# Kernel tuning notes

Hardware: AMD Instinct MI355X
Metric: run time of the kernel (lower is better)

Reference implementation:

```python
import jax, jax.numpy as jnp
import numpy as np

BN_EPS = 1e-5
STRIDE = 12          # ACCENT_DOWNSAMPLE_STRIDE
NQ = 8               # ACCENT_VQ_QUANTIZERS
K = 256              # ACCENT_VQ_CODEBOOK_SIZE
VQ_D = 16            # ACCENT_VQ_DIM
EMB = 128            # ACCENT_EMBEDDING_DIM


def conv1d(x, w, b, stride=1, padding=0):
    # x: (B, Cin, T), w: (Cout, Cin, Kw)
    y = jax.lax.conv_general_dilated(
        x, w, window_strides=(stride,), padding=[(padding, padding)],
        dimension_numbers=("NCW", "OIW", "NCW"))
    return y + b[None, :, None]


def batchnorm(x, gamma, beta, mean, var):
    # eval-mode BatchNorm1d over channel dim
    inv = jax.lax.rsqrt(var + BN_EPS)
    return (x - mean[None, :, None]) * (inv * gamma)[None, :, None] + beta[None, :, None]


def setup_inputs() -> dict:
    key = jax.random.key(0)
    ks = jax.random.split(key, 12)
    C = 256
    d = {
        "mel_spectrogram": jax.random.normal(ks[0], (16, 80, 4096), jnp.float32),
        "w1": jax.random.normal(ks[1], (C, 80, 5), jnp.float32) * 0.05,
        "b1": jnp.zeros((C,), jnp.float32),
        "g1": jnp.ones((C,), jnp.float32),
        "be1": jnp.zeros((C,), jnp.float32),
        "m1": jax.random.normal(ks[2], (C,), jnp.float32) * 0.1,
        "v1": jax.random.uniform(ks[3], (C,), jnp.float32, 0.5, 1.5),
        "w2": jax.random.normal(ks[4], (C, C, 5), jnp.float32) * 0.03,
        "b2": jnp.zeros((C,), jnp.float32),
        "g2": jnp.ones((C,), jnp.float32),
        "be2": jnp.zeros((C,), jnp.float32),
        "m2": jax.random.normal(ks[5], (C,), jnp.float32) * 0.1,
        "v2": jax.random.uniform(ks[6], (C,), jnp.float32, 0.5, 1.5),
        "wd": jax.random.normal(ks[7], (EMB, C, 2 * STRIDE), jnp.float32) * 0.02,
        "bd": jnp.zeros((EMB,), jnp.float32),
        "wp": jax.random.normal(ks[8], (VQ_D, EMB, 1), jnp.float32) * 0.1,
        "bp": jnp.zeros((VQ_D,), jnp.float32),
        "codebooks": jax.random.normal(ks[9], (NQ, K, VQ_D), jnp.float32) * 0.3,
    }
    return d


def reference(mel_spectrogram, w1, b1, g1, be1, m1, v1,
              w2, b2, g2, be2, m2, v2, wd, bd, wp, bp, codebooks):
    # CNN stack
    x = jax.nn.relu(batchnorm(conv1d(mel_spectrogram, w1, b1, 1, 2), g1, be1, m1, v1))
    x = jax.nn.relu(batchnorm(conv1d(x, w2, b2, 1, 2), g2, be2, m2, v2))
    # Downsample conv: kernel=24, stride=12, pad=6
    e_a_unq = conv1d(x, wd, bd, STRIDE, STRIDE // 2)          # (B, 128, T')
    z = conv1d(e_a_unq, wp, bp, 1, 0)                          # (B, 16, T')
    # RVQ: 8 sequential cdist-argmin-subtract steps
    r = jnp.transpose(z, (0, 2, 1))                            # (B, T', 16)
    idx_list = []
    for q in range(NQ):
        cb = codebooks[q]                                      # (K, 16)
        # squared euclidean distances (B, T', K)
        d = (jnp.sum(r * r, -1, keepdims=True)
             - 2.0 * jnp.einsum("btd,kd->btk", r, cb)
             + jnp.sum(cb * cb, -1))
        idx = jnp.argmin(d, axis=-1)                           # (B, T')
        idx_list.append(idx)
        r = r - cb[idx]                                        # residual update
    indices = jnp.stack(idx_list, axis=0)                      # (NQ, B, T')
    return e_a_unq, indices
```

## Files before the change

kernel.cpp:

```cpp
#include <hip/hip_runtime.h>
#include <math.h>

#define B_    16
#define T_    4096
#define C_    256
#define CIN1  80
#define EMB   128
#define TP    341
#define NPOS  (B_*TP)
#define NQ_   8
#define KCB   256
#define BN_EPS 1e-5

__global__ __launch_bounds__(256) void prep_v7(
    const float* __restrict__ w2, const float* __restrict__ wd,
    const float* __restrict__ b1, const float* __restrict__ g1,
    const float* __restrict__ be1, const float* __restrict__ m1,
    const float* __restrict__ v1,
    const float* __restrict__ b2, const float* __restrict__ g2,
    const float* __restrict__ be2, const float* __restrict__ m2,
    const float* __restrict__ v2,
    float* __restrict__ w2t, float* __restrict__ wdt,
    double* __restrict__ a1, double* __restrict__ bt1,
    double* __restrict__ a2, double* __restrict__ bt2)
{
    int j = blockIdx.x * 256 + threadIdx.x;
    if (j < 256*24*128) wdt[j] = wd[(size_t)(j & 127) * 6144 + (j >> 7)];
    if (j < 256*5*256)  w2t[j] = w2[(size_t)(j & 255) * 1280 + (j >> 8)];
    if (j < 256) {
        double inv1 = 1.0 / sqrt((double)v1[j] + BN_EPS);
        double s1 = (double)g1[j] * inv1;
        a1[j]  = s1;
        bt1[j] = ((double)b1[j] - (double)m1[j]) * s1 + (double)be1[j];
        double inv2 = 1.0 / sqrt((double)v2[j] + BN_EPS);
        double s2 = (double)g2[j] * inv2;
        a2[j]  = s2;
        bt2[j] = ((double)b2[j] - (double)m2[j]) * s2 + (double)be2[j];
    }
}

__device__ __forceinline__ int swz_pair(int col) {
    int bw = col >> 1;
    return ((bw ^ ((bw >> 3) & 7)) << 1);
}
__device__ __forceinline__ int swz_scalar(int col) {
    int bw = col >> 1;
    return (((bw ^ ((bw >> 3) & 7)) << 1) | (col & 1));
}

template<int CIN, typename Tin, bool TR>
__global__ __launch_bounds__(256, 2) void conv5_v8(
    const Tin* __restrict__ in,
    const float* __restrict__ wt,
    const double* __restrict__ alpha, const double* __restrict__ beta,
    double* __restrict__ out)
{
    const int b   = blockIdx.z;
    const int co0 = blockIdx.y * 64;
    const int t0  = blockIdx.x * 256;
    const int tid = threadIdx.x;
    const int tcol = tid & 15;
    const int trow = tid >> 4;

    __shared__ __align__(16) double xs[8][264];
    __shared__ __align__(16) double wsh[40][64];

    double acc[4][16];
    #pragma unroll
    for (int i = 0; i < 4; ++i)
        #pragma unroll
        for (int j = 0; j < 16; ++j) acc[i][j] = 0.0;

    for (int c0 = 0; c0 < CIN; c0 += 8) {
        for (int i = tid; i < 8 * 260; i += 256) {
            int ci = i / 260, col = i - ci * 260;
            int t = t0 - 2 + col;
            double v = 0.0;
            if (t >= 0 && t < T_) v = (double)in[((size_t)(b * CIN + c0 + ci)) * T_ + t];
            xs[ci][swz_scalar(col)] = v;
        }
        for (int i = tid; i < 40 * 64; i += 256) {
            int r = i >> 6, co = i & 63;
            float wv;
            if (TR) wv = wt[(size_t)(c0 * 5 + r) * 256 + co0 + co];
            else    wv = wt[(size_t)(co0 + co) * (CIN * 5) + c0 * 5 + r];
            wsh[r][co] = (double)wv;
        }
        __syncthreads();

        #pragma unroll 2
        for (int ci = 0; ci < 8; ++ci) {
            double wv[20];
            #pragma unroll
            for (int k = 0; k < 5; ++k) {
                double2 wa = *(const double2*)&wsh[ci * 5 + k][trow * 4];
                double2 wb = *(const double2*)&wsh[ci * 5 + k][trow * 4 + 2];
                wv[k * 4 + 0] = wa.x; wv[k * 4 + 1] = wa.y;
                wv[k * 4 + 2] = wb.x; wv[k * 4 + 3] = wb.y;
            }
            #pragma unroll
            for (int h = 0; h < 2; ++h) {
                double xv[12];
                #pragma unroll
                for (int m = 0; m < 6; ++m) {
                    double2 v2 = *(const double2*)&xs[ci][swz_pair(tcol * 16 + h * 8 + 2 * m)];
                    xv[2 * m] = v2.x; xv[2 * m + 1] = v2.y;
                }
                #pragma unroll
                for (int k = 0; k < 5; ++k)
                    #pragma unroll
                    for (int i4 = 0; i4 < 4; ++i4) {
                        double w = wv[k * 4 + i4];
                        #pragma unroll
                        for (int j = 0; j < 8; ++j)
                            acc[i4][h * 8 + j] = fma(w, xv[j + k], acc[i4][h * 8 + j]);
                    }
            }
        }
        __syncthreads();
    }

    const int cobase = co0 + trow * 4;
    const int tg = t0 + tcol * 16;
    #pragma unroll
    for (int i4 = 0; i4 < 4; ++i4) {
        double a = alpha[cobase + i4], bt = beta[cobase + i4];
        size_t base = ((size_t)(b * C_ + cobase + i4)) * T_ + tg;
        #pragma unroll
        for (int m = 0; m < 8; ++m) {
            double2 o;
            double y0 = fma(acc[i4][2 * m], a, bt);
            double y1 = fma(acc[i4][2 * m + 1], a, bt);
            o.x = y0 > 0.0 ? y0 : 0.0;
            o.y = y1 > 0.0 ? y1 : 0.0;
            *(double2*)&out[base + 2 * m] = o;
        }
    }
}

__global__ __launch_bounds__(256, 2) void convd_f64_v7(
    const double* __restrict__ x2,
    const float* __restrict__ wdt,
    double* __restrict__ parts,
    int nb, int nsplit, int cis)
{
    const int bz  = blockIdx.z;
    const int s   = bz % nsplit;
    const int b   = bz / nsplit;
    const int tp0 = blockIdx.x * 128;
    const int tid = threadIdx.x;
    const int tcol = tid & 15;
    const int crow = tid >> 4;

    __shared__ __align__(16) double xs2[24][132];
    __shared__ __align__(16) double wsh[24][128];

    double acc[8][8];
    #pragma unroll
    for (int i = 0; i < 8; ++i)
        #pragma unroll
        for (int j = 0; j < 8; ++j) acc[i][j] = 0.0;

    const int tbase = tp0 * 12 - 6;
    const int ci_begin = s * cis;

    for (int c = ci_begin; c < ci_begin + cis; ++c) {
        for (int i = tid; i < 1548; i += 256) {
            int t = tbase + i;
            double v = (t >= 0 && t < T_)
                ? x2[((size_t)(b * 256 + c)) * T_ + t] : 0.0;
            int tp = (i * 43691) >> 19;
            int kp = i - tp * 12;
            xs2[kp][swz_scalar(tp)] = v;
            if (tp >= 1) xs2[kp + 12][swz_scalar(tp - 1)] = v;
        }
        for (int i = tid; i < 24 * 128; i += 256) {
            int r = i >> 7, cc = i & 127;
            wsh[r][cc] = (double)wdt[((size_t)c * 24 + r) * 128 + cc];
        }
        __syncthreads();

        #pragma unroll 4
        for (int k = 0; k < 24; ++k) {
            double wv[8];
            #pragma unroll
            for (int m = 0; m < 4; ++m) {
                double2 w2v = *(const double2*)&wsh[k][crow * 8 + 2 * m];
                wv[2 * m] = w2v.x; wv[2 * m + 1] = w2v.y;
            }
            #pragma unroll
            for (int jp = 0; jp < 4; ++jp) {
                double2 xp = *(const double2*)&xs2[k][swz_pair(tcol * 2 + 32 * jp)];
                #pragma unroll
                for (int i = 0; i < 8; ++i) {
                    acc[i][jp * 2]     = fma(wv[i], xp.x, acc[i][jp * 2]);
                    acc[i][jp * 2 + 1] = fma(wv[i], xp.y, acc[i][jp * 2 + 1]);
                }
            }
        }
        __syncthreads();
    }

    #pragma unroll
    for (int i = 0; i < 8; ++i) {
        int co = crow * 8 + i;
        #pragma unroll
        for (int jp = 0; jp < 4; ++jp) {
            #pragma unroll
            for (int e = 0; e < 2; ++e) {
                int tp = tp0 + tcol * 2 + 32 * jp + e;
                if (tp < TP)
                    parts[(((size_t)s * nb + b) * EMB + co) * TP + tp] = acc[i][jp * 2 + e];
            }
        }
    }
}

__global__ __launch_bounds__(256) void convd_combine(
    double* __restrict__ parts,
    const float* __restrict__ bd,
    float* __restrict__ e_out,
    int nb, int b_off, int nsplit)
{
    int idx = blockIdx.x * 256 + threadIdx.x;
    int total = nb * EMB * TP;
    if (idx >= total) return;
    int rem = idx % (EMB * TP);
    int co = rem / TP;
    size_t stride = (size_t)nb * EMB * TP;
    double y = 0.0;
    for (int s = 0; s < nsplit; ++s)
        y += parts[(size_t)s * stride + idx];
    y += (double)bd[co];
    parts[idx] = y;
    e_out[(size_t)b_off * EMB * TP + idx] = (float)y;
}

__global__ __launch_bounds__(128) void zproj_f64(
    const double* __restrict__ ed,
    const float* __restrict__ wp,
    const float* __restrict__ bp,
    double* __restrict__ z)
{
    const int b = blockIdx.y;
    const int t = blockIdx.x * 128 + threadIdx.x;
    __shared__ double wps[16][128];
    for (int i = threadIdx.x; i < 16 * 128; i += 128)
        wps[i >> 7][i & 127] = (double)wp[i];
    __syncthreads();
    if (t >= TP) return;
    double acc[16];
    #pragma unroll
    for (int v = 0; v < 16; ++v) acc[v] = (double)bp[v];
    for (int co = 0; co < 128; ++co) {
        double x = ed[((size_t)(b * EMB + co)) * TP + t];
        #pragma unroll
        for (int v = 0; v < 16; ++v) acc[v] = fma(x, wps[v][co], acc[v]);
    }
    #pragma unroll
    for (int v = 0; v < 16; ++v)
        z[((size_t)(b * TP + t)) * 16 + v] = acc[v];
}

__global__ __launch_bounds__(256) void rvq_f64_v2(
    const double* __restrict__ z,
    const float* __restrict__ cb,
    float* __restrict__ out_idx)
{
    const int pos = blockIdx.x;
    const int tid = threadIdx.x;
    const int lane = tid & 63;
    const int wv = tid >> 6;

    __shared__ double r[16];
    __shared__ double wd_s[4];
    __shared__ int wi_s[4];
    __shared__ int best_s;

    if (tid < 16) r[tid] = z[(size_t)pos * 16 + tid];
    __syncthreads();

    for (int q = 0; q < NQ_; ++q) {
        const float* c = cb + ((size_t)(q * KCB) + tid) * 16;
        double d = 0.0;
        #pragma unroll
        for (int i = 0; i < 16; ++i) {
            double diff = r[i] - (double)c[i];
            d = fma(diff, diff, d);
        }
        int idx = tid;
        #pragma unroll
        for (int sft = 32; sft > 0; sft >>= 1) {
            double d2 = __shfl_down(d, sft, 64);
            int i2 = __shfl_down(idx, sft, 64);
            if (d2 < d || (d2 == d && i2 < idx)) { d = d2; idx = i2; }
        }
        if (lane == 0) { wd_s[wv] = d; wi_s[wv] = idx; }
        __syncthreads();
        if (tid == 0) {
            double bd_ = wd_s[0]; int bi = wi_s[0];
            #pragma unroll
            for (int w = 1; w < 4; ++w) {
                if (wd_s[w] < bd_ || (wd_s[w] == bd_ && wi_s[w] < bi)) {
                    bd_ = wd_s[w]; bi = wi_s[w];
                }
            }
            best_s = bi;
            out_idx[(size_t)q * NPOS + pos] = (float)bi;
        }
        __syncthreads();
        int best = best_s;
        if (tid < 16)
            r[tid] = r[tid] - (double)cb[((size_t)(q * KCB) + best) * 16 + tid];
        __syncthreads();
    }
}

extern "C" void kernel_launch(void* const* d_in, const int* in_sizes, int n_in,
                              void* d_out, int out_size, void* d_ws, size_t ws_size,
                              hipStream_t stream) {
    const float* mel = (const float*)d_in[0];
    const float* w1  = (const float*)d_in[1];
    const float* b1  = (const float*)d_in[2];
    const float* g1  = (const float*)d_in[3];
    const float* be1 = (const float*)d_in[4];
    const float* m1  = (const float*)d_in[5];
    const float* v1  = (const float*)d_in[6];
    const float* w2  = (const float*)d_in[7];
    const float* b2  = (const float*)d_in[8];
    const float* g2  = (const float*)d_in[9];
    const float* be2 = (const float*)d_in[10];
    const float* m2  = (const float*)d_in[11];
    const float* v2  = (const float*)d_in[12];
    const float* wd  = (const float*)d_in[13];
    const float* bd  = (const float*)d_in[14];
    const float* wp  = (const float*)d_in[15];
    const float* bp  = (const float*)d_in[16];
    const float* cb  = (const float*)d_in[17];

    const int nb = 8;
    const int ngrp = B_ / nb;
    const int nsplit = 16;
    const int cis = 256 / nsplit;

    auto al = [](size_t x) { return (x + 255) & ~(size_t)255; };
    const size_t x1_big   = (size_t)nb * C_ * T_ * 8;
    const size_t x1_small = (size_t)4  * C_ * T_ * 8;
    const size_t parts_b  = (size_t)nsplit * nb * EMB * TP * 8;
    const size_t x2_bytes = (size_t)nb * C_ * T_ * 8;
    const size_t tail = al((size_t)256*5*256*4)
                      + al((size_t)256*24*128*4)
                      + 4 * al(2048)
                      + al((size_t)B_ * TP * 16 * 8);
    const size_t need_big = al(x1_big) + al(x2_bytes) + tail;

    const bool big = (ws_size >= need_big);
    const int cc = big ? 8 : 4;
    const size_t shared_bytes = big ? x1_big
                                    : (x1_small > parts_b ? x1_small : parts_b);

    char* ws = (char*)d_ws;
    size_t off = 0;
    auto alloc = [&](size_t bytes) -> char* {
        char* p = ws + off;
        off = (off + bytes + 255) & ~(size_t)255;
        return p;
    };
    char* shared = alloc(shared_bytes);
    double* x1d  = (double*)shared;
    double* parts= (double*)shared;
    double* x2d  = (double*)alloc(x2_bytes);
    float*  w2t  = (float*)alloc((size_t)256*5*256*4);
    float*  wdt  = (float*)alloc((size_t)256*24*128*4);
    double* a1d  = (double*)alloc(2048);
    double* bt1d = (double*)alloc(2048);
    double* a2d  = (double*)alloc(2048);
    double* bt2d = (double*)alloc(2048);
    double* zd   = (double*)alloc((size_t)B_ * TP * 16 * 8);

    float* e_out   = (float*)d_out;
    float* idx_out = (float*)d_out + (size_t)B_ * EMB * TP;

    prep_v7<<<3072, 256, 0, stream>>>(w2, wd, b1, g1, be1, m1, v1,
                                      b2, g2, be2, m2, v2,
                                      w2t, wdt, a1d, bt1d, a2d, bt2d);

    const int comb_blocks = (nb * EMB * TP + 255) / 256;
    for (int g = 0; g < ngrp; ++g) {
        for (int ch = 0; ch < nb / cc; ++ch) {
            int b_abs = g * nb + ch * cc;
            conv5_v8<CIN1, float, false>
                <<<dim3(16, 4, cc), 256, 0, stream>>>(
                mel + (size_t)b_abs * CIN1 * T_, w1, a1d, bt1d,
                x1d + (big ? (size_t)ch * cc * C_ * T_ : 0));
            conv5_v8<C_, double, true>
                <<<dim3(16, 4, cc), 256, 0, stream>>>(
                x1d + (big ? (size_t)ch * cc * C_ * T_ : 0), w2t, a2d, bt2d,
                x2d + (size_t)ch * cc * C_ * T_);
        }
        convd_f64_v7<<<dim3(3, 1, nb * nsplit), 256, 0, stream>>>(
            x2d, wdt, parts, nb, nsplit, cis);
        convd_combine<<<comb_blocks, 256, 0, stream>>>(
            parts, bd, e_out, nb, g * nb, nsplit);
        zproj_f64<<<dim3(3, nb), 128, 0, stream>>>(
            parts, wp, bp, zd + (size_t)g * nb * TP * 16);
    }
    rvq_f64_v2<<<NPOS, 256, 0, stream>>>(zd, cb, idx_out);
}
```

Before: 1.781 ms.

## Rewrite conv5 as register-tiled direct-from-global kernel with wave-uniform weights

Replaces the LDS-tiled fp64 conv5 kernel with one that keeps no shared memory. Each wave handles 16 output channels and each lane two time steps, reading inputs straight from global memory. Weights are loaded as wave-uniform (scalar) values from a pre-transposed, optionally fp64-converted copy, so the inner loop avoids per-iteration conversion. The change also raises occupancy to 4 blocks per CU, drops the batch chunking so each conv covers all 8 batches in one launch, and adds a tier that stores weights as double when workspace allows. The cost is less data reuse per thread and heavier reliance on cache for the overlapping input reads.

```diff
diff --git a/kernel.cpp b/kernel.cpp
--- a/kernel.cpp
+++ b/kernel.cpp
@@ -12,21 +12,20 @@
 #define KCB   256
 #define BN_EPS 1e-5
 
-__global__ __launch_bounds__(256) void prep_v7(
-    const float* __restrict__ w2, const float* __restrict__ wd,
+__global__ __launch_bounds__(256) void prep_common(
+    const float* __restrict__ wd,
     const float* __restrict__ b1, const float* __restrict__ g1,
     const float* __restrict__ be1, const float* __restrict__ m1,
     const float* __restrict__ v1,
     const float* __restrict__ b2, const float* __restrict__ g2,
     const float* __restrict__ be2, const float* __restrict__ m2,
     const float* __restrict__ v2,
-    float* __restrict__ w2t, float* __restrict__ wdt,
+    float* __restrict__ wdt,
     double* __restrict__ a1, double* __restrict__ bt1,
     double* __restrict__ a2, double* __restrict__ bt2)
 {
     int j = blockIdx.x * 256 + threadIdx.x;
     if (j < 256*24*128) wdt[j] = wd[(size_t)(j & 127) * 6144 + (j >> 7)];
-    if (j < 256*5*256)  w2t[j] = w2[(size_t)(j & 255) * 1280 + (j >> 8)];
     if (j < 256) {
         double inv1 = 1.0 / sqrt((double)v1[j] + BN_EPS);
         double s1 = (double)g1[j] * inv1;
@@ -39,6 +38,23 @@
     }
 }
 
+__global__ __launch_bounds__(256) void prep_wf64(
+    const float* __restrict__ w1, const float* __restrict__ w2,
+    double* __restrict__ w1td, double* __restrict__ w2td)
+{
+    int j = blockIdx.x * 256 + threadIdx.x;
+    if (j < 256*5*256) w2td[j] = (double)w2[(size_t)(j & 255) * 1280 + (j >> 8)];
+    if (j < 80*5*256)  w1td[j] = (double)w1[(size_t)(j & 255) * 400 + (j >> 8)];
+}
+__global__ __launch_bounds__(256) void prep_wf32(
+    const float* __restrict__ w1, const float* __restrict__ w2,
+    float* __restrict__ w1tf, float* __restrict__ w2tf)
+{
+    int j = blockIdx.x * 256 + threadIdx.x;
+    if (j < 256*5*256) w2tf[j] = w2[(size_t)(j & 255) * 1280 + (j >> 8)];
+    if (j < 80*5*256)  w1tf[j] = w1[(size_t)(j & 255) * 400 + (j >> 8)];
+}
+
 __device__ __forceinline__ int swz_pair(int col) {
     int bw = col >> 1;
     return ((bw ^ ((bw >> 3) & 7)) << 1);
@@ -48,93 +64,62 @@
     return (((bw ^ ((bw >> 3) & 7)) << 1) | (col & 1));
 }
 
-template<int CIN, typename Tin, bool TR>
-__global__ __launch_bounds__(256, 2) void conv5_v8(
+template<int CIN, typename Tin, typename WT>
+__global__ __launch_bounds__(256, 4) void conv5_v10(
     const Tin* __restrict__ in,
-    const float* __restrict__ wt,
+    const WT* __restrict__ wt,
     const double* __restrict__ alpha, const double* __restrict__ beta,
     double* __restrict__ out)
 {
-    const int b   = blockIdx.z;
-    const int co0 = blockIdx.y * 64;
-    const int t0  = blockIdx.x * 256;
-    const int tid = threadIdx.x;
-    const int tcol = tid & 15;
-    const int trow = tid >> 4;
-
-    __shared__ __align__(16) double xs[8][264];
-    __shared__ __align__(16) double wsh[40][64];
-
-    double acc[4][16];
-    #pragma unroll
-    for (int i = 0; i < 4; ++i)
-        #pragma unroll
-        for (int j = 0; j < 16; ++j) acc[i][j] = 0.0;
-
-    for (int c0 = 0; c0 < CIN; c0 += 8) {
-        for (int i = tid; i < 8 * 260; i += 256) {
-            int ci = i / 260, col = i - ci * 260;
-            int t = t0 - 2 + col;
-            double v = 0.0;
-            if (t >= 0 && t < T_) v = (double)in[((size_t)(b * CIN + c0 + ci)) * T_ + t];
-            xs[ci][swz_scalar(col)] = v;
-        }
-        for (int i = tid; i < 40 * 64; i += 256) {
-            int r = i >> 6, co = i & 63;
-            float wv;
-            if (TR) wv = wt[(size_t)(c0 * 5 + r) * 256 + co0 + co];
-            else    wv = wt[(size_t)(co0 + co) * (CIN * 5) + c0 * 5 + r];
-            wsh[r][co] = (double)wv;
-        }
-        __syncthreads();
-
-        #pragma unroll 2
-        for (int ci = 0; ci < 8; ++ci) {
-            double wv[20];
-            #pragma unroll
-            for (int k = 0; k < 5; ++k) {
-                double2 wa = *(const double2*)&wsh[ci * 5 + k][trow * 4];
-                double2 wb = *(const double2*)&wsh[ci * 5 + k][trow * 4 + 2];
-                wv[k * 4 + 0] = wa.x; wv[k * 4 + 1] = wa.y;
-                wv[k * 4 + 2] = wb.x; wv[k * 4 + 3] = wb.y;
-            }
-            #pragma unroll
-            for (int h = 0; h < 2; ++h) {
-                double xv[12];
-                #pragma unroll
-                for (int m = 0; m < 6; ++m) {
-                    double2 v2 = *(const double2*)&xs[ci][swz_pair(tcol * 16 + h * 8 + 2 * m)];
-                    xv[2 * m] = v2.x; xv[2 * m + 1] = v2.y;
-                }
-                #pragma unroll
-                for (int k = 0; k < 5; ++k)
-                    #pragma unroll
-                    for (int i4 = 0; i4 < 4; ++i4) {
-                        double w = wv[k * 4 + i4];
-                        #pragma unroll
-                        for (int j = 0; j < 8; ++j)
-                            acc[i4][h * 8 + j] = fma(w, xv[j + k], acc[i4][h * 8 + j]);
-                    }
-            }
-        }
-        __syncthreads();
-    }
-
-    const int cobase = co0 + trow * 4;
-    const int tg = t0 + tcol * 16;
-    #pragma unroll
-    for (int i4 = 0; i4 < 4; ++i4) {
-        double a = alpha[cobase + i4], bt = beta[cobase + i4];
-        size_t base = ((size_t)(b * C_ + cobase + i4)) * T_ + tg;
-        #pragma unroll
-        for (int m = 0; m < 8; ++m) {
-            double2 o;
-            double y0 = fma(acc[i4][2 * m], a, bt);
-            double y1 = fma(acc[i4][2 * m + 1], a, bt);
-            o.x = y0 > 0.0 ? y0 : 0.0;
-            o.y = y1 > 0.0 ? y1 : 0.0;
-            *(double2*)&out[base + 2 * m] = o;
-        }
+    const int b  = blockIdx.z;
+    const int t0 = blockIdx.y * 128;
+    const int wv = __builtin_amdgcn_readfirstlane((int)(threadIdx.x >> 6));
+    const int lane = threadIdx.x & 63;
+    const int co0 = blockIdx.x * 64 + wv * 16;
+    const int t = t0 + lane * 2;
+
+    double acc[16][2];
+    #pragma unroll
+    for (int c = 0; c < 16; ++c) { acc[c][0] = 0.0; acc[c][1] = 0.0; }
+
+    const Tin* xb = in + (size_t)b * CIN * T_;
+    const bool interior = (t0 != 0) && (t0 + 130 <= T_);
+
+    for (int ci = 0; ci < CIN; ++ci) {
+        double xv[6];
+        const Tin* xp = xb + (size_t)ci * T_ + (t - 2);
+        if (interior) {
+            #pragma unroll
+            for (int d = 0; d < 6; ++d) xv[d] = (double)xp[d];
+        } else {
+            #pragma unroll
+            for (int d = 0; d < 6; ++d) {
+                int tt = t - 2 + d;
+                xv[d] = (tt >= 0 && tt < T_) ? (double)xp[d] : 0.0;
+            }
+        }
+        const WT* wrow = wt + (size_t)ci * 5 * 256 + co0;
+        #pragma unroll
+        for (int k = 0; k < 5; ++k) {
+            #pragma unroll
+            for (int c = 0; c < 16; ++c) {
+                double w = (double)wrow[k * 256 + c];
+                acc[c][0] = fma(w, xv[k],     acc[c][0]);
+                acc[c][1] = fma(w, xv[k + 1], acc[c][1]);
+            }
+        }
+    }
+
+    #pragma unroll
+    for (int c = 0; c < 16; ++c) {
+        int co = co0 + c;
+        double a = alpha[co], bt = beta[co];
+        double y0 = fma(acc[c][0], a, bt);
+        double y1 = fma(acc[c][1], a, bt);
+        double2 o;
+        o.x = y0 > 0.0 ? y0 : 0.0;
+        o.y = y1 > 0.0 ? y1 : 0.0;
+        *(double2*)&out[((size_t)(b * C_ + co)) * T_ + t] = o;
     }
 }
 
@@ -343,21 +328,14 @@
     const int nsplit = 16;
     const int cis = 256 / nsplit;
 
-    auto al = [](size_t x) { return (x + 255) & ~(size_t)255; };
-    const size_t x1_big   = (size_t)nb * C_ * T_ * 8;
-    const size_t x1_small = (size_t)4  * C_ * T_ * 8;
-    const size_t parts_b  = (size_t)nsplit * nb * EMB * TP * 8;
+    const size_t x1_bytes = (size_t)nb * C_ * T_ * 8;
     const size_t x2_bytes = (size_t)nb * C_ * T_ * 8;
-    const size_t tail = al((size_t)256*5*256*4)
-                      + al((size_t)256*24*128*4)
-                      + 4 * al(2048)
-                      + al((size_t)B_ * TP * 16 * 8);
-    const size_t need_big = al(x1_big) + al(x2_bytes) + tail;
-
-    const bool big = (ws_size >= need_big);
-    const int cc = big ? 8 : 4;
-    const size_t shared_bytes = big ? x1_big
-                                    : (x1_small > parts_b ? x1_small : parts_b);
+    const size_t zd_bytes = (size_t)B_ * TP * 16 * 8;
+
+    const size_t needA = x1_bytes + x2_bytes + (size_t)80*5*256*8
+                       + (size_t)256*5*256*8 + (size_t)256*24*128*4
+                       + 4*2048 + zd_bytes + 8192;
+    const bool tierA = (ws_size >= needA);
 
     char* ws = (char*)d_ws;
     size_t off = 0;
@@ -366,37 +344,43 @@
         off = (off + bytes + 255) & ~(size_t)255;
         return p;
     };
-    char* shared = alloc(shared_bytes);
+    char* shared = alloc(x1_bytes);
     double* x1d  = (double*)shared;
     double* parts= (double*)shared;
     double* x2d  = (double*)alloc(x2_bytes);
-    float*  w2t  = (float*)alloc((size_t)256*5*256*4);
+    void*   w1t  = (void*)alloc(tierA ? (size_t)80*5*256*8  : (size_t)80*5*256*4);
+    void*   w2t  = (void*)alloc(tierA ? (size_t)256*5*256*8 : (size_t)256*5*256*4);
     float*  wdt  = (float*)alloc((size_t)256*24*128*4);
     double* a1d  = (double*)alloc(2048);
     double* bt1d = (double*)alloc(2048);
     double* a2d  = (double*)alloc(2048);
     double* bt2d = (double*)alloc(2048);
-    double* zd   = (double*)alloc((size_t)B_ * TP * 16 * 8);
+    double* zd   = (double*)alloc(zd_bytes);
 
     float* e_out   = (float*)d_out;
     float* idx_out = (float*)d_out + (size_t)B_ * EMB * TP;
 
-    prep_v7<<<3072, 256, 0, stream>>>(w2, wd, b1, g1, be1, m1, v1,
-                                      b2, g2, be2, m2, v2,
-                                      w2t, wdt, a1d, bt1d, a2d, bt2d);
+    prep_common<<<3072, 256, 0, stream>>>(wd, b1, g1, be1, m1, v1,
+                                          b2, g2, be2, m2, v2,
+                                          wdt, a1d, bt1d, a2d, bt2d);
+    if (tierA)
+        prep_wf64<<<1280, 256, 0, stream>>>(w1, w2, (double*)w1t, (double*)w2t);
+    else
+        prep_wf32<<<1280, 256, 0, stream>>>(w1, w2, (float*)w1t, (float*)w2t);
 
     const int comb_blocks = (nb * EMB * TP + 255) / 256;
     for (int g = 0; g < ngrp; ++g) {
-        for (int ch = 0; ch < nb / cc; ++ch) {
-            int b_abs = g * nb + ch * cc;
-            conv5_v8<CIN1, float, false>
-                <<<dim3(16, 4, cc), 256, 0, stream>>>(
-                mel + (size_t)b_abs * CIN1 * T_, w1, a1d, bt1d,
-                x1d + (big ? (size_t)ch * cc * C_ * T_ : 0));
-            conv5_v8<C_, double, true>
-                <<<dim3(16, 4, cc), 256, 0, stream>>>(
-                x1d + (big ? (size_t)ch * cc * C_ * T_ : 0), w2t, a2d, bt2d,
-                x2d + (size_t)ch * cc * C_ * T_);
+        const float* mel_g = mel + (size_t)(g * nb) * CIN1 * T_;
+        if (tierA) {
+            conv5_v10<CIN1, float, double><<<dim3(4, 32, nb), 256, 0, stream>>>(
+                mel_g, (const double*)w1t, a1d, bt1d, x1d);
+            conv5_v10<C_, double, double><<<dim3(4, 32, nb), 256, 0, stream>>>(
+                x1d, (const double*)w2t, a2d, bt2d, x2d);
+        } else {
+            conv5_v10<CIN1, float, float><<<dim3(4, 32, nb), 256, 0, stream>>>(
+                mel_g, (const float*)w1t, a1d, bt1d, x1d);
+            conv5_v10<C_, double, float><<<dim3(4, 32, nb), 256, 0, stream>>>(
+                x1d, (const float*)w2t, a2d, bt2d, x2d);
         }
         convd_f64_v7<<<dim3(3, 1, nb * nsplit), 256, 0, stream>>>(
             x2d, wdt, parts, nb, nsplit, cis);
```

After: 1.926 ms. 1.08x slower.
